# Kernel tuning notes

Measured on AMD Instinct MI355X. Metric: run time of the kernel, lower is better.

The kernel has to match this reference:

```python
import jax, jax.numpy as jnp
import numpy as np

NUM_HEADS = 12
WINDOW = (14, 14)


def gen_relative_position_index(ws):
    num_rel = (2 * ws[0] - 1) * (2 * ws[1] - 1) + 3
    coords = np.stack(np.meshgrid(np.arange(ws[0]), np.arange(ws[1]), indexing='ij'))
    cf = coords.reshape(2, -1)  # [2, Wh*Ww]
    rel = cf[:, :, None] - cf[:, None, :]  # [2, A, A]
    rel = rel.transpose(1, 2, 0).astype(np.int64)  # [A, A, 2]
    rel[..., 0] += ws[0] - 1
    rel[..., 1] += ws[1] - 1
    rel[..., 0] *= 2 * ws[1] - 1
    area = ws[0] * ws[1]
    idx = np.zeros((area + 1, area + 1), dtype=np.int64)
    idx[1:, 1:] = rel.sum(-1)
    idx[0, :] = num_rel - 3
    idx[:, 0] = num_rel - 2
    idx[0, 0] = num_rel - 1
    return idx


def setup_inputs() -> dict:
    key = jax.random.key(0)
    ks = jax.random.split(key, 7)
    B, N, C = 128, WINDOW[0] * WINDOW[1] + 1, 768
    num_rel = (2 * WINDOW[0] - 1) * (2 * WINDOW[1] - 1) + 3  # 732
    s = 0.02
    return {
        'x': jax.random.normal(ks[0], (B, N, C), jnp.float32),
        'qkv_w': jax.random.normal(ks[1], (3 * C, C), jnp.float32) * s,
        'q_bias': jax.random.normal(ks[2], (C,), jnp.float32) * s,
        'v_bias': jax.random.normal(ks[3], (C,), jnp.float32) * s,
        'rel_pos_table': jax.random.normal(ks[4], (num_rel, NUM_HEADS), jnp.float32) * s,
        'proj_w': jax.random.normal(ks[5], (C, C), jnp.float32) * s,
        'proj_b': jax.random.normal(ks[6], (C,), jnp.float32) * s,
        'rel_index': jnp.asarray(gen_relative_position_index(WINDOW)),
    }


def reference(x, qkv_w, q_bias, v_bias, rel_pos_table, proj_w, proj_b, rel_index):
    B, N, C = x.shape
    H = NUM_HEADS
    hd = C // H
    scale = hd ** -0.5
    # qkv projection with (q_bias, zeros, v_bias) composite bias
    bias = jnp.concatenate([q_bias, jnp.zeros_like(q_bias), v_bias])
    qkv = x @ qkv_w.T + bias  # [B, N, 3C]
    qkv = qkv.reshape(B, N, 3, H, hd).transpose(2, 0, 3, 1, 4)  # [3, B, H, N, hd]
    q, k, v = qkv[0], qkv[1], qkv[2]
    # gather relative position bias: [N, N, H] -> [H, N, N]
    rel_bias = rel_pos_table[rel_index.reshape(-1)].reshape(N, N, H).transpose(2, 0, 1)
    attn = jnp.einsum('bhnd,bhmd->bhnm', q * scale, k) + rel_bias[None]
    attn = jax.nn.softmax(attn, axis=-1)
    out = jnp.einsum('bhnm,bhmd->bhnd', attn, v)  # [B, H, N, hd]
    out = out.transpose(0, 2, 1, 3).reshape(B, N, C)
    return out @ proj_w.T + proj_b
```

## Files before the change

kernel.cpp:

```cpp
#include <hip/hip_runtime.h>

typedef unsigned short u16;
typedef __attribute__((ext_vector_type(8))) short short8;
typedef __attribute__((ext_vector_type(8))) __bf16 bf16x8;
typedef __attribute__((ext_vector_type(4))) float floatx4;

#define BATCH 128
#define SEQ 197
#define CH 768
#define NH 12
#define HD 64
#define MROWS (BATCH * SEQ)

__device__ __forceinline__ floatx4 mfma16(short8 a, short8 b, floatx4 c) {
  return __builtin_amdgcn_mfma_f32_16x16x32_bf16(
      __builtin_bit_cast(bf16x8, a), __builtin_bit_cast(bf16x8, b), c, 0, 0, 0);
}

__device__ __forceinline__ u16 f2bf(float f) {
  unsigned u = __builtin_bit_cast(unsigned, f);
  return (u16)((u + 0x7fffu + ((u >> 16) & 1u)) >> 16);
}

__device__ __forceinline__ void async16(const u16* g, u16* s) {
  __builtin_amdgcn_global_load_lds((const __attribute__((address_space(1))) void*)g,
                                   (__attribute__((address_space(3))) void*)s, 16, 0, 0);
}

__global__ __launch_bounds__(256) void preproc(const float4* __restrict__ x, ushort4* __restrict__ xo, int n0,
                                               const float4* __restrict__ w1, ushort4* __restrict__ w1o, int n1,
                                               const float4* __restrict__ w2, ushort4* __restrict__ w2o, int n2,
                                               const int* __restrict__ idx, const float* __restrict__ table,
                                               float* __restrict__ relb) {
  int i = blockIdx.x * 256 + threadIdx.x;
  const float4* in; ushort4* out; int j;
  if (i < n0) { in = x; out = xo; j = i; }
  else if (i < n0 + n1) { in = w1; out = w1o; j = i - n0; }
  else if (i < n0 + n1 + n2) { in = w2; out = w2o; j = i - n0 - n1; }
  else {
    int t = i - (n0 + n1 + n2);
    if (t < SEQ * SEQ) {
      int id = idx[t];
      const float* row = table + id * NH;
#pragma unroll
      for (int h = 0; h < NH; h++) relb[h * (SEQ * SEQ) + t] = row[h];
    }
    return;
  }
  float4 v = in[j];
  ushort4 o;
  o.x = f2bf(v.x); o.y = f2bf(v.y); o.z = f2bf(v.z); o.w = f2bf(v.w);
  out[j] = o;
}

__global__ __launch_bounds__(256, 2) void gemm_qkv(const u16* __restrict__ A,
                                                   const u16* __restrict__ W,
                                                   const float* __restrict__ qb,
                                                   const float* __restrict__ vb,
                                                   u16* __restrict__ q_buf,
                                                   u16* __restrict__ k_buf,
                                                   u16* __restrict__ v_buf) {
  __shared__ u16 S[2][(128 + 256) * 32];
  const int BUF = (128 + 256) * 32;
  const int BOFF = 128 * 32;
  int tid = threadIdx.x;
  int wave = tid >> 6, lane = tid & 63, quad = lane >> 4, c16 = lane & 15;
  int wm = wave >> 1, wn = wave & 1;

  int nwg = gridDim.x;
  int orig = blockIdx.x;
  int xcd = orig & 7, pos = orig >> 3;
  int qq = nwg >> 3, rr = nwg & 7;
  int lid = (xcd < rr ? xcd * (qq + 1) : rr * (qq + 1) + (xcd - rr) * qq) + pos;
  int mblk = lid / 9, nblk = lid - mblk * 9;
  int m0 = mblk * 128, n0 = nblk * 256;

  int lrow = lane >> 2;
  int lcol = (((lane & 3) ^ ((lane >> 3) & 3))) * 8;
  const u16* Ag0 = A + (size_t)(m0 + wave * 32 + lrow) * CH + lcol;
  const u16* Ag1 = Ag0 + (size_t)16 * CH;
  const u16* Bg0 = W + (size_t)(n0 + wave * 64 + lrow) * CH + lcol;
  const u16* Bg1 = Bg0 + (size_t)16 * CH;
  const u16* Bg2 = Bg0 + (size_t)32 * CH;
  const u16* Bg3 = Bg0 + (size_t)48 * CH;
  int aw0 = (wave * 32) * 32;
  int aw1 = (wave * 32 + 16) * 32;
  int bw0 = BOFF + (wave * 64) * 32;
  int bw1 = BOFF + (wave * 64 + 16) * 32;
  int bw2 = BOFF + (wave * 64 + 32) * 32;
  int bw3 = BOFF + (wave * 64 + 48) * 32;
  int fsl = (quad ^ ((c16 >> 1) & 3)) * 8;
  int aro = (wm * 64 + c16) * 32 + fsl;
  int bro = BOFF + (wn * 128 + c16) * 32 + fsl;

  floatx4 acc[4][8] = {};
  u16* sbase = &S[0][0];

  async16(Ag0, sbase + aw0);
  async16(Ag1, sbase + aw1);
  async16(Bg0, sbase + bw0);
  async16(Bg1, sbase + bw1);
  async16(Bg2, sbase + bw2);
  async16(Bg3, sbase + bw3);
  asm volatile("s_waitcnt vmcnt(0)" ::: "memory");
  __builtin_amdgcn_s_barrier();
  asm volatile("" ::: "memory");

  int cur = 0;
  for (int kt = 1; kt < CH / 32; ++kt) {
    int kk = kt * 32;
    u16* sn = sbase + (cur ^ 1) * BUF;
    async16(Ag0 + kk, sn + aw0);
    async16(Ag1 + kk, sn + aw1);
    async16(Bg0 + kk, sn + bw0);
    async16(Bg1 + kk, sn + bw1);
    async16(Bg2 + kk, sn + bw2);
    async16(Bg3 + kk, sn + bw3);
    const u16* sc = sbase + cur * BUF;
    short8 af[4], bfr[8];
#pragma unroll
    for (int i = 0; i < 4; i++) af[i] = *(const short8*)(sc + aro + i * 16 * 32);
#pragma unroll
    for (int j = 0; j < 8; j++) bfr[j] = *(const short8*)(sc + bro + j * 16 * 32);
#pragma unroll
    for (int i = 0; i < 4; i++)
#pragma unroll
      for (int j = 0; j < 8; j++) acc[i][j] = mfma16(af[i], bfr[j], acc[i][j]);
    asm volatile("s_waitcnt vmcnt(0)" ::: "memory");
    __builtin_amdgcn_s_barrier();
    asm volatile("" ::: "memory");
    cur ^= 1;
  }
  {
    const u16* sc = sbase + cur * BUF;
    short8 af[4], bfr[8];
#pragma unroll
    for (int i = 0; i < 4; i++) af[i] = *(const short8*)(sc + aro + i * 16 * 32);
#pragma unroll
    for (int j = 0; j < 8; j++) bfr[j] = *(const short8*)(sc + bro + j * 16 * 32);
#pragma unroll
    for (int i = 0; i < 4; i++)
#pragma unroll
      for (int j = 0; j < 8; j++) acc[i][j] = mfma16(af[i], bfr[j], acc[i][j]);
  }

#pragma unroll
  for (int j = 0; j < 8; j++) {
    int gcol = n0 + wn * 128 + j * 16 + c16;
    int t = gcol / CH;
    int rem = gcol - t * CH;
    int h = rem >> 6, d = rem & 63;
    float badd = (t == 0) ? qb[rem] : (t == 2 ? vb[rem] : 0.0f);
    u16* dst = (t == 0) ? q_buf : (t == 1 ? k_buf : v_buf);
#pragma unroll
    for (int i = 0; i < 4; i++) {
#pragma unroll
      for (int r = 0; r < 4; r++) {
        int grow = m0 + wm * 64 + i * 16 + quad * 4 + r;
        int bb = grow / SEQ;
        int n = grow - bb * SEQ;
        dst[(((size_t)bb * NH + h) * SEQ + n) * HD + d] = f2bf(acc[i][j][r] + badd);
      }
    }
  }
}

#define PS 232
#define VS 264

__global__ __launch_bounds__(256, 2) void attn(const u16* __restrict__ q_buf,
                                               const u16* __restrict__ k_buf,
                                               const u16* __restrict__ v_buf,
                                               const float* __restrict__ relb,
                                               u16* __restrict__ attn_out) {
  __shared__ u16 Vt[64 * VS];
  __shared__ u16 P[4 * 16 * PS];

  int h = blockIdx.x, b = blockIdx.y;
  int tid = threadIdx.x, wave = tid >> 6, lane = tid & 63, quad = lane >> 4, c16 = lane & 15;
  size_t bh = (size_t)b * NH + h;
  const u16* Q = q_buf + bh * SEQ * HD;
  const u16* Kp = k_buf + bh * SEQ * HD;
  const u16* Vp = v_buf + bh * SEQ * HD;
  const float* RB = relb + (size_t)h * (SEQ * SEQ);

  {
    int mrow = tid >> 3, dbase = (tid & 7) * 8;
#pragma unroll
    for (int i = 0; i < 7; i++) {
      int m = mrow + 32 * i;
      if (m < SEQ) {
        ushort4 v0 = *(const ushort4*)(Vp + m * HD + dbase);
        ushort4 v1 = *(const ushort4*)(Vp + m * HD + dbase + 4);
        Vt[(dbase + 0) * VS + m] = v0.x;
        Vt[(dbase + 1) * VS + m] = v0.y;
        Vt[(dbase + 2) * VS + m] = v0.z;
        Vt[(dbase + 3) * VS + m] = v0.w;
        Vt[(dbase + 4) * VS + m] = v1.x;
        Vt[(dbase + 5) * VS + m] = v1.y;
        Vt[(dbase + 6) * VS + m] = v1.z;
        Vt[(dbase + 7) * VS + m] = v1.w;
      } else {
#pragma unroll
        for (int dd = 0; dd < 8; dd++) Vt[(dbase + dd) * VS + m] = 0;
      }
    }
  }
  __syncthreads();

  u16* Pw = P + wave * 16 * PS;
  for (int rt = wave; rt < 13; rt += 4) {
    int q0 = rt * 16;
    int qr = min(q0 + c16, SEQ - 1);
    short8 qa0 = *(const short8*)(Q + qr * HD + quad * 8);
    short8 qa1 = *(const short8*)(Q + qr * HD + 32 + quad * 8);

    floatx4 sacc[13];
#pragma unroll
    for (int nt = 0; nt < 13; nt++) {
      int mc = min(nt * 16 + c16, SEQ - 1);
      floatx4 a = {0.f, 0.f, 0.f, 0.f};
      a = mfma16(qa0, *(const short8*)(Kp + mc * HD + quad * 8), a);
      a = mfma16(qa1, *(const short8*)(Kp + mc * HD + 32 + quad * 8), a);
      sacc[nt] = a;
    }

#pragma unroll
    for (int r = 0; r < 4; r++) {
      int rq = min(q0 + quad * 4 + r, SEQ - 1);
      const float* RBr = RB + (size_t)rq * SEQ;
      float mx = -1e30f;
#pragma unroll
      for (int nt = 0; nt < 13; nt++) {
        int m = nt * 16 + c16;
        float s = -1e30f;
        if (m < SEQ) s = sacc[nt][r] * 0.125f + RBr[m];
        sacc[nt][r] = s;
        mx = fmaxf(mx, s);
      }
      mx = fmaxf(mx, __shfl_xor(mx, 1));
      mx = fmaxf(mx, __shfl_xor(mx, 2));
      mx = fmaxf(mx, __shfl_xor(mx, 4));
      mx = fmaxf(mx, __shfl_xor(mx, 8));
      float sum = 0.f;
#pragma unroll
      for (int nt = 0; nt < 13; nt++) {
        float e = __expf(sacc[nt][r] - mx);
        sacc[nt][r] = e;
        sum += e;
      }
      sum += __shfl_xor(sum, 1);
      sum += __shfl_xor(sum, 2);
      sum += __shfl_xor(sum, 4);
      sum += __shfl_xor(sum, 8);
      float inv = 1.f / sum;
      int prow = (quad * 4 + r) * PS;
#pragma unroll
      for (int nt = 0; nt < 13; nt++)
        Pw[prow + nt * 16 + c16] = f2bf(sacc[nt][r] * inv);
      Pw[prow + 208 + c16] = 0;
    }

    floatx4 oacc[4] = {};
#pragma unroll
    for (int ks = 0; ks < 7; ks++) {
      short8 a = *(const short8*)(Pw + c16 * PS + ks * 32 + quad * 8);
#pragma unroll
      for (int dt = 0; dt < 4; dt++) {
        short8 bb = *(const short8*)(Vt + (dt * 16 + c16) * VS + ks * 32 + quad * 8);
        oacc[dt] = mfma16(a, bb, oacc[dt]);
      }
    }
#pragma unroll
    for (int dt = 0; dt < 4; dt++) {
      int d = dt * 16 + c16;
#pragma unroll
      for (int r = 0; r < 4; r++) {
        int grow = q0 + quad * 4 + r;
        if (grow < SEQ)
          attn_out[((size_t)b * SEQ + grow) * CH + h * HD + d] = f2bf(oacc[dt][r]);
      }
    }
  }
}

__global__ __launch_bounds__(256, 2) void gemm_proj(const u16* __restrict__ A,
                                                    const u16* __restrict__ W,
                                                    const float* __restrict__ bias,
                                                    float* __restrict__ out) {
  __shared__ u16 S[2][(128 + 256) * 32];
  const int BUF = (128 + 256) * 32;
  const int BOFF = 128 * 32;
  int tid = threadIdx.x;
  int wave = tid >> 6, lane = tid & 63, quad = lane >> 4, c16 = lane & 15;
  int wm = wave >> 1, wn = wave & 1;

  int nwg = gridDim.x;
  int orig = blockIdx.x;
  int xcd = orig & 7, pos = orig >> 3;
  int qq = nwg >> 3, rr = nwg & 7;
  int lid = (xcd < rr ? xcd * (qq + 1) : rr * (qq + 1) + (xcd - rr) * qq) + pos;
  int mblk = lid / 3, nblk = lid - mblk * 3;
  int m0 = mblk * 128, n0 = nblk * 256;

  int lrow = lane >> 2;
  int lcol = (((lane & 3) ^ ((lane >> 3) & 3))) * 8;
  const u16* Ag0 = A + (size_t)(m0 + wave * 32 + lrow) * CH + lcol;
  const u16* Ag1 = Ag0 + (size_t)16 * CH;
  const u16* Bg0 = W + (size_t)(n0 + wave * 64 + lrow) * CH + lcol;
  const u16* Bg1 = Bg0 + (size_t)16 * CH;
  const u16* Bg2 = Bg0 + (size_t)32 * CH;
  const u16* Bg3 = Bg0 + (size_t)48 * CH;
  int aw0 = (wave * 32) * 32;
  int aw1 = (wave * 32 + 16) * 32;
  int bw0 = BOFF + (wave * 64) * 32;
  int bw1 = BOFF + (wave * 64 + 16) * 32;
  int bw2 = BOFF + (wave * 64 + 32) * 32;
  int bw3 = BOFF + (wave * 64 + 48) * 32;
  int fsl = (quad ^ ((c16 >> 1) & 3)) * 8;
  int aro = (wm * 64 + c16) * 32 + fsl;
  int bro = BOFF + (wn * 128 + c16) * 32 + fsl;

  floatx4 acc[4][8] = {};
  u16* sbase = &S[0][0];

  async16(Ag0, sbase + aw0);
  async16(Ag1, sbase + aw1);
  async16(Bg0, sbase + bw0);
  async16(Bg1, sbase + bw1);
  async16(Bg2, sbase + bw2);
  async16(Bg3, sbase + bw3);
  asm volatile("s_waitcnt vmcnt(0)" ::: "memory");
  __builtin_amdgcn_s_barrier();
  asm volatile("" ::: "memory");

  int cur = 0;
  for (int kt = 1; kt < CH / 32; ++kt) {
    int kk = kt * 32;
    u16* sn = sbase + (cur ^ 1) * BUF;
    async16(Ag0 + kk, sn + aw0);
    async16(Ag1 + kk, sn + aw1);
    async16(Bg0 + kk, sn + bw0);
    async16(Bg1 + kk, sn + bw1);
    async16(Bg2 + kk, sn + bw2);
    async16(Bg3 + kk, sn + bw3);
    const u16* sc = sbase + cur * BUF;
    short8 af[4], bfr[8];
#pragma unroll
    for (int i = 0; i < 4; i++) af[i] = *(const short8*)(sc + aro + i * 16 * 32);
#pragma unroll
    for (int j = 0; j < 8; j++) bfr[j] = *(const short8*)(sc + bro + j * 16 * 32);
#pragma unroll
    for (int i = 0; i < 4; i++)
#pragma unroll
      for (int j = 0; j < 8; j++) acc[i][j] = mfma16(af[i], bfr[j], acc[i][j]);
    asm volatile("s_waitcnt vmcnt(0)" ::: "memory");
    __builtin_amdgcn_s_barrier();
    asm volatile("" ::: "memory");
    cur ^= 1;
  }
  {
    const u16* sc = sbase + cur * BUF;
    short8 af[4], bfr[8];
#pragma unroll
    for (int i = 0; i < 4; i++) af[i] = *(const short8*)(sc + aro + i * 16 * 32);
#pragma unroll
    for (int j = 0; j < 8; j++) bfr[j] = *(const short8*)(sc + bro + j * 16 * 32);
#pragma unroll
    for (int i = 0; i < 4; i++)
#pragma unroll
      for (int j = 0; j < 8; j++) acc[i][j] = mfma16(af[i], bfr[j], acc[i][j]);
  }

#pragma unroll
  for (int j = 0; j < 8; j++) {
    int gcol = n0 + wn * 128 + j * 16 + c16;
    float bj = bias[gcol];
#pragma unroll
    for (int i = 0; i < 4; i++)
#pragma unroll
      for (int r = 0; r < 4; r++) {
        int grow = m0 + wm * 64 + i * 16 + quad * 4 + r;
        out[(size_t)grow * CH + gcol] = acc[i][j][r] + bj;
      }
  }
}

extern "C" void kernel_launch(void* const* d_in, const int* in_sizes, int n_in,
                              void* d_out, int out_size, void* d_ws, size_t ws_size,
                              hipStream_t stream) {
  const float* x      = (const float*)d_in[0];
  const float* qkv_w  = (const float*)d_in[1];
  const float* q_bias = (const float*)d_in[2];
  const float* v_bias = (const float*)d_in[3];
  const float* table  = (const float*)d_in[4];
  const float* proj_w = (const float*)d_in[5];
  const float* proj_b = (const float*)d_in[6];
  const int*   rel_ix = (const int*)d_in[7];
  float* out = (float*)d_out;

  char* ws = (char*)d_ws;
  size_t off = 0;
  u16* x_bf  = (u16*)(ws + off); off += (size_t)MROWS * CH * 2;
  u16* wq_bf = (u16*)(ws + off); off += (size_t)3 * CH * CH * 2;
  u16* wp_bf = (u16*)(ws + off); off += (size_t)CH * CH * 2;
  u16* q_buf = (u16*)(ws + off); off += (size_t)MROWS * CH * 2;
  u16* k_buf = (u16*)(ws + off); off += (size_t)MROWS * CH * 2;
  u16* v_buf = (u16*)(ws + off); off += (size_t)MROWS * CH * 2;
  u16* ao_bf = (u16*)(ws + off); off += (size_t)MROWS * CH * 2;
  float* relb = (float*)(ws + off);

  int n0 = MROWS * CH / 4;
  int n1 = 3 * CH * CH / 4;
  int n2 = CH * CH / 4;
  int ntot = n0 + n1 + n2 + SEQ * SEQ;
  preproc<<<(ntot + 255) / 256, 256, 0, stream>>>(
      (const float4*)x, (ushort4*)x_bf, n0,
      (const float4*)qkv_w, (ushort4*)wq_bf, n1,
      (const float4*)proj_w, (ushort4*)wp_bf, n2,
      rel_ix, table, relb);
  gemm_qkv<<<dim3(197 * 9), 256, 0, stream>>>(x_bf, wq_bf, q_bias, v_bias, q_buf, k_buf, v_buf);
  attn<<<dim3(NH, BATCH), 256, 0, stream>>>(q_buf, k_buf, v_buf, relb, ao_bf);
  gemm_proj<<<dim3(197 * 3), 256, 0, stream>>>(ao_bf, wp_bf, proj_b, out);
}
```

Before: 402.6 us.

## Triple-buffer GEMM LDS pipeline and raise wave priority around attention MFMAs

Measured after the change: 385.1 us. 4.3% less time.

```diff
diff --git a/kernel.cpp b/kernel.cpp
--- a/kernel.cpp
+++ b/kernel.cpp
@@ -60,9 +60,10 @@
                                                    u16* __restrict__ q_buf,
                                                    u16* __restrict__ k_buf,
                                                    u16* __restrict__ v_buf) {
-  __shared__ u16 S[2][(128 + 256) * 32];
+  __shared__ u16 S[3][(128 + 256) * 32];
   const int BUF = (128 + 256) * 32;
   const int BOFF = 128 * 32;
+  const int NT = CH / 32;
   int tid = threadIdx.x;
   int wave = tid >> 6, lane = tid & 63, quad = lane >> 4, c16 = lane & 15;
   int wm = wave >> 1, wn = wave & 1;
@@ -96,53 +97,55 @@
   floatx4 acc[4][8] = {};
   u16* sbase = &S[0][0];
 
-  async16(Ag0, sbase + aw0);
-  async16(Ag1, sbase + aw1);
-  async16(Bg0, sbase + bw0);
-  async16(Bg1, sbase + bw1);
-  async16(Bg2, sbase + bw2);
-  async16(Bg3, sbase + bw3);
+#define STAGE(kk_, sn_)                                                        \
+  do {                                                                         \
+    async16(Ag0 + (kk_), (sn_) + aw0);                                         \
+    async16(Ag1 + (kk_), (sn_) + aw1);                                         \
+    async16(Bg0 + (kk_), (sn_) + bw0);                                         \
+    async16(Bg1 + (kk_), (sn_) + bw1);                                         \
+    async16(Bg2 + (kk_), (sn_) + bw2);                                         \
+    async16(Bg3 + (kk_), (sn_) + bw3);                                         \
+  } while (0)
+
+#define COMPUTE(sc_)                                                           \
+  do {                                                                         \
+    const u16* sc = (sc_);                                                     \
+    short8 af[4], bfr[8];                                                      \
+    _Pragma("unroll")                                                          \
+    for (int i = 0; i < 4; i++) af[i] = *(const short8*)(sc + aro + i * 16 * 32); \
+    _Pragma("unroll")                                                          \
+    for (int j = 0; j < 8; j++) bfr[j] = *(const short8*)(sc + bro + j * 16 * 32); \
+    _Pragma("unroll")                                                          \
+    for (int i = 0; i < 4; i++)                                                \
+      _Pragma("unroll")                                                        \
+      for (int j = 0; j < 8; j++) acc[i][j] = mfma16(af[i], bfr[j], acc[i][j]); \
+  } while (0)
+
+  STAGE(0, sbase);
+  STAGE(32, sbase + BUF);
+  asm volatile("s_waitcnt vmcnt(6)" ::: "memory");
+  __builtin_amdgcn_s_barrier();
+  asm volatile("" ::: "memory");
+
+  int cc = 0, ss = 2;
+  for (int kt = 0; kt < NT - 2; ++kt) {
+    STAGE((kt + 2) * 32, sbase + ss * BUF);
+    COMPUTE(sbase + cc * BUF);
+    asm volatile("s_waitcnt vmcnt(6)" ::: "memory");
+    __builtin_amdgcn_s_barrier();
+    asm volatile("" ::: "memory");
+    cc = cc == 2 ? 0 : cc + 1;
+    ss = ss == 2 ? 0 : ss + 1;
+  }
+  COMPUTE(sbase + cc * BUF);
   asm volatile("s_waitcnt vmcnt(0)" ::: "memory");
   __builtin_amdgcn_s_barrier();
   asm volatile("" ::: "memory");
-
-  int cur = 0;
-  for (int kt = 1; kt < CH / 32; ++kt) {
-    int kk = kt * 32;
-    u16* sn = sbase + (cur ^ 1) * BUF;
-    async16(Ag0 + kk, sn + aw0);
-    async16(Ag1 + kk, sn + aw1);
-    async16(Bg0 + kk, sn + bw0);
-    async16(Bg1 + kk, sn + bw1);
-    async16(Bg2 + kk, sn + bw2);
-    async16(Bg3 + kk, sn + bw3);
-    const u16* sc = sbase + cur * BUF;
-    short8 af[4], bfr[8];
-#pragma unroll
-    for (int i = 0; i < 4; i++) af[i] = *(const short8*)(sc + aro + i * 16 * 32);
-#pragma unroll
-    for (int j = 0; j < 8; j++) bfr[j] = *(const short8*)(sc + bro + j * 16 * 32);
-#pragma unroll
-    for (int i = 0; i < 4; i++)
-#pragma unroll
-      for (int j = 0; j < 8; j++) acc[i][j] = mfma16(af[i], bfr[j], acc[i][j]);
-    asm volatile("s_waitcnt vmcnt(0)" ::: "memory");
-    __builtin_amdgcn_s_barrier();
-    asm volatile("" ::: "memory");
-    cur ^= 1;
-  }
-  {
-    const u16* sc = sbase + cur * BUF;
-    short8 af[4], bfr[8];
-#pragma unroll
-    for (int i = 0; i < 4; i++) af[i] = *(const short8*)(sc + aro + i * 16 * 32);
-#pragma unroll
-    for (int j = 0; j < 8; j++) bfr[j] = *(const short8*)(sc + bro + j * 16 * 32);
-#pragma unroll
-    for (int i = 0; i < 4; i++)
-#pragma unroll
-      for (int j = 0; j < 8; j++) acc[i][j] = mfma16(af[i], bfr[j], acc[i][j]);
-  }
+  cc = cc == 2 ? 0 : cc + 1;
+  COMPUTE(sbase + cc * BUF);
+
+#undef STAGE
+#undef COMPUTE
 
 #pragma unroll
   for (int j = 0; j < 8; j++) {
@@ -216,6 +219,7 @@
     short8 qa1 = *(const short8*)(Q + qr * HD + 32 + quad * 8);
 
     floatx4 sacc[13];
+    __builtin_amdgcn_s_setprio(1);
 #pragma unroll
     for (int nt = 0; nt < 13; nt++) {
       int mc = min(nt * 16 + c16, SEQ - 1);
@@ -224,6 +228,7 @@
       a = mfma16(qa1, *(const short8*)(Kp + mc * HD + 32 + quad * 8), a);
       sacc[nt] = a;
     }
+    __builtin_amdgcn_s_setprio(0);
 
 #pragma unroll
     for (int r = 0; r < 4; r++) {
@@ -262,6 +267,7 @@
     }
 
     floatx4 oacc[4] = {};
+    __builtin_amdgcn_s_setprio(1);
 #pragma unroll
     for (int ks = 0; ks < 7; ks++) {
       short8 a = *(const short8*)(Pw + c16 * PS + ks * 32 + quad * 8);
@@ -271,6 +277,7 @@
         oacc[dt] = mfma16(a, bb, oacc[dt]);
       }
     }
+    __builtin_amdgcn_s_setprio(0);
 #pragma unroll
     for (int dt = 0; dt < 4; dt++) {
       int d = dt * 16 + c16;
@@ -288,9 +295,10 @@
                                                     const u16* __restrict__ W,
                                                     const float* __restrict__ bias,
                                                     float* __restrict__ out) {
-  __shared__ u16 S[2][(128 + 256) * 32];
+  __shared__ u16 S[3][(128 + 256) * 32];
   const int BUF = (128 + 256) * 32;
   const int BOFF = 128 * 32;
+  const int NT = CH / 32;
   int tid = threadIdx.x;
   int wave = tid >> 6, lane = tid & 63, quad = lane >> 4, c16 = lane & 15;
   int wm = wave >> 1, wn = wave & 1;
@@ -324,53 +332,55 @@
   floatx4 acc[4][8] = {};
   u16* sbase = &S[0][0];
 
-  async16(Ag0, sbase + aw0);
-  async16(Ag1, sbase + aw1);
-  async16(Bg0, sbase + bw0);
-  async16(Bg1, sbase + bw1);
-  async16(Bg2, sbase + bw2);
-  async16(Bg3, sbase + bw3);
+#define STAGE(kk_, sn_)                                                        \
+  do {                                                                         \
+    async16(Ag0 + (kk_), (sn_) + aw0);                                         \
+    async16(Ag1 + (kk_), (sn_) + aw1);                                         \
+    async16(Bg0 + (kk_), (sn_) + bw0);                                         \
+    async16(Bg1 + (kk_), (sn_) + bw1);                                         \
+    async16(Bg2 + (kk_), (sn_) + bw2);                                         \
+    async16(Bg3 + (kk_), (sn_) + bw3);                                         \
+  } while (0)
+
+#define COMPUTE(sc_)                                                           \
+  do {                                                                         \
+    const u16* sc = (sc_);                                                     \
+    short8 af[4], bfr[8];                                                      \
+    _Pragma("unroll")                                                          \
+    for (int i = 0; i < 4; i++) af[i] = *(const short8*)(sc + aro + i * 16 * 32); \
+    _Pragma("unroll")                                                          \
+    for (int j = 0; j < 8; j++) bfr[j] = *(const short8*)(sc + bro + j * 16 * 32); \
+    _Pragma("unroll")                                                          \
+    for (int i = 0; i < 4; i++)                                                \
+      _Pragma("unroll")                                                        \
+      for (int j = 0; j < 8; j++) acc[i][j] = mfma16(af[i], bfr[j], acc[i][j]); \
+  } while (0)
+
+  STAGE(0, sbase);
+  STAGE(32, sbase + BUF);
+  asm volatile("s_waitcnt vmcnt(6)" ::: "memory");
+  __builtin_amdgcn_s_barrier();
+  asm volatile("" ::: "memory");
+
+  int cc = 0, ss = 2;
+  for (int kt = 0; kt < NT - 2; ++kt) {
+    STAGE((kt + 2) * 32, sbase + ss * BUF);
+    COMPUTE(sbase + cc * BUF);
+    asm volatile("s_waitcnt vmcnt(6)" ::: "memory");
+    __builtin_amdgcn_s_barrier();
+    asm volatile("" ::: "memory");
+    cc = cc == 2 ? 0 : cc + 1;
+    ss = ss == 2 ? 0 : ss + 1;
+  }
+  COMPUTE(sbase + cc * BUF);
   asm volatile("s_waitcnt vmcnt(0)" ::: "memory");
   __builtin_amdgcn_s_barrier();
   asm volatile("" ::: "memory");
-
-  int cur = 0;
-  for (int kt = 1; kt < CH / 32; ++kt) {
-    int kk = kt * 32;
-    u16* sn = sbase + (cur ^ 1) * BUF;
-    async16(Ag0 + kk, sn + aw0);
-    async16(Ag1 + kk, sn + aw1);
-    async16(Bg0 + kk, sn + bw0);
-    async16(Bg1 + kk, sn + bw1);
-    async16(Bg2 + kk, sn + bw2);
-    async16(Bg3 + kk, sn + bw3);
-    const u16* sc = sbase + cur * BUF;
-    short8 af[4], bfr[8];
-#pragma unroll
-    for (int i = 0; i < 4; i++) af[i] = *(const short8*)(sc + aro + i * 16 * 32);
-#pragma unroll
-    for (int j = 0; j < 8; j++) bfr[j] = *(const short8*)(sc + bro + j * 16 * 32);
-#pragma unroll
-    for (int i = 0; i < 4; i++)
-#pragma unroll
-      for (int j = 0; j < 8; j++) acc[i][j] = mfma16(af[i], bfr[j], acc[i][j]);
-    asm volatile("s_waitcnt vmcnt(0)" ::: "memory");
-    __builtin_amdgcn_s_barrier();
-    asm volatile("" ::: "memory");
-    cur ^= 1;
-  }
-  {
-    const u16* sc = sbase + cur * BUF;
-    short8 af[4], bfr[8];
-#pragma unroll
-    for (int i = 0; i < 4; i++) af[i] = *(const short8*)(sc + aro + i * 16 * 32);
-#pragma unroll
-    for (int j = 0; j < 8; j++) bfr[j] = *(const short8*)(sc + bro + j * 16 * 32);
-#pragma unroll
-    for (int i = 0; i < 4; i++)
-#pragma unroll
-      for (int j = 0; j < 8; j++) acc[i][j] = mfma16(af[i], bfr[j], acc[i][j]);
-  }
+  cc = cc == 2 ? 0 : cc + 1;
+  COMPUTE(sbase + cc * BUF);
+
+#undef STAGE
+#undef COMPUTE
 
 #pragma unroll
   for (int j = 0; j < 8; j++) {
```
